# Optimization experiments

Measured on AMD Instinct MI355X. Metric: run time of the kernel, lower is better.

The kernel has to match this reference:

```python
import jax, jax.numpy as jnp
import numpy as np

B = 8            # number of point clouds in the batch
NT = 8192        # target points per cloud
NS = 2048        # source points per cloud
K = 3            # knn_interpolate neighbors
C_TGT = 128      # target (skip) feature channels
C_SRC = 256      # source feature channels
C_IN = C_TGT + C_SRC   # 384 = mlp_channels[0]
C_HID = 256            # mlp_channels[1]
C_OUT = 128            # mlp_channels[2]
EPS = 1e-16


def setup_inputs() -> dict:
    key = jax.random.key(0)
    ks = jax.random.split(key, 10)
    Nt, Ns = B * NT, B * NS
    s1 = 1.0 / np.sqrt(C_IN)
    s2 = 1.0 / np.sqrt(C_HID)
    return {
        "x_target": jax.random.normal(ks[0], (Nt, C_TGT), jnp.float32),
        "pos_target": jax.random.normal(ks[1], (Nt, 3), jnp.float32),
        "batch_target": (jnp.arange(Nt, dtype=jnp.int32) // NT).astype(jnp.int32),
        "x_source": jax.random.normal(ks[2], (Ns, C_SRC), jnp.float32),
        "pos_source": jax.random.normal(ks[3], (Ns, 3), jnp.float32),
        "batch_source": (jnp.arange(Ns, dtype=jnp.int32) // NS).astype(jnp.int32),
        "W1": jax.random.normal(ks[4], (C_IN, C_HID), jnp.float32) * s1,
        "b1": jnp.zeros((C_HID,), jnp.float32),
        "W2": jax.random.normal(ks[5], (C_HID, C_OUT), jnp.float32) * s2,
        "b2": jnp.zeros((C_OUT,), jnp.float32),
        "Ws": jax.random.normal(ks[6], (C_IN, C_OUT), jnp.float32) * s1,
        "bs": jnp.zeros((C_OUT,), jnp.float32),
    }


def _knn_interpolate(x_source, pos_source, pos_target):
    """PyG knn_interpolate with inverse-squared-distance weights.
    Batches are contiguous equal-size blocks -> reshape to [B, N, ...]."""
    pt = pos_target.reshape(B, NT, 3)
    ps = pos_source.reshape(B, NS, 3)
    xs = x_source.reshape(B, NS, C_SRC)
    # squared pairwise distances [B, NT, NS]
    d2 = jnp.sum((pt[:, :, None, :] - ps[:, None, :, :]) ** 2, axis=-1)
    neg, idx = jax.lax.top_k(-d2, K)            # idx: [B, NT, K]
    w = 1.0 / jnp.clip(-neg, EPS)               # inverse squared distance
    gathered = jax.vmap(lambda x, i: x[i])(xs, idx)  # [B, NT, K, C_SRC]
    interp = jnp.sum(w[..., None] * gathered, axis=2) / jnp.sum(w, axis=2)[..., None]
    return interp.reshape(B * NT, C_SRC)


def reference(x_target, pos_target, batch_target, x_source, pos_source,
              batch_source, W1, b1, W2, b2, Ws, bs):
    interpolated = _knn_interpolate(x_source, pos_source, pos_target)
    combined = jnp.concatenate([x_target, interpolated], axis=1)  # [Nt, 384]
    h = jax.nn.relu(combined @ W1 + b1) @ W2 + b2                 # MLP branch
    res = combined @ Ws + bs                                      # shortcut
    return jax.nn.relu(h + res)
```

## Files before the change

kernel.cpp:

```cpp
#include <hip/hip_runtime.h>
#include <hip/hip_bf16.h>

#define B_    8
#define NT_   8192
#define NS_   2048
#define NTOT  (B_ * NT_)
#define CTGT  128
#define CSRC  256
#define CIN   384
#define CHID  256
#define COUT  128

typedef __bf16 bf16x8 __attribute__((ext_vector_type(8)));
typedef float  f32x4  __attribute__((ext_vector_type(4)));
typedef unsigned short u16x8 __attribute__((ext_vector_type(8)));

__device__ inline unsigned short f2bf(float f) {
    unsigned int u = __float_as_uint(f);
    u += 0x7FFF + ((u >> 16) & 1);
    return (unsigned short)(u >> 16);
}

__device__ __forceinline__ void gload16(const unsigned short* g, unsigned short* l) {
    __builtin_amdgcn_global_load_lds(
        (const __attribute__((address_space(1))) unsigned int*)g,
        (__attribute__((address_space(3))) unsigned int*)l, 16, 0, 0);
}

__device__ __forceinline__ void stage_ab(
    const unsigned short* __restrict__ ga, int ldA,
    const unsigned short* __restrict__ gb, int ldB,
    unsigned short* Alds, unsigned short* Blds,
    int k0, int widu, int lane) {
    int rloc = lane >> 2;
    int cswz = ((lane & 3) ^ ((lane >> 3) & 3)) * 8;
#pragma unroll
    for (int i = 0; i < 2; ++i) {
        int c = widu * 2 + i;
        int row = c * 16 + rloc;
        gload16(ga + (size_t)row * ldA + k0 + cswz, Alds + c * 512);
        gload16(gb + (size_t)row * ldB + k0 + cswz, Blds + c * 512);
    }
}

__global__ __launch_bounds__(256) void prep_weights(
    const float* __restrict__ W1, const float* __restrict__ Ws,
    const float* __restrict__ W2,
    unsigned short* __restrict__ Wct, unsigned short* __restrict__ W2t) {
    int g = blockIdx.x * 256 + threadIdx.x;
    if (g < CIN * CIN) {
        int n = g / CIN, k = g % CIN;
        float v = (n < CHID) ? W1[(size_t)k * CHID + n]
                             : Ws[(size_t)k * COUT + (n - CHID)];
        Wct[g] = f2bf(v);
    } else {
        int g2 = g - CIN * CIN;
        if (g2 < COUT * CHID) {
            int n = g2 / CHID, k = g2 % CHID;
            W2t[g2] = f2bf(W2[(size_t)k * COUT + n]);
        }
    }
}

__global__ __launch_bounds__(256) void knn_kernel(
    const float* __restrict__ pos_t, const float* __restrict__ pos_s,
    int* __restrict__ knn_i, float* __restrict__ knn_d) {
    __shared__ float4 ps4[NS_];
    __shared__ float  md[256 * 3];
    __shared__ int    mi[256 * 3];

    int blk = blockIdx.x;
    int batch = blk >> 8;
    const float* src = pos_s + (size_t)batch * NS_ * 3;
    for (int i = threadIdx.x; i < NS_; i += 256) {
        ps4[i] = make_float4(src[i * 3 + 0], src[i * 3 + 1], src[i * 3 + 2], 0.0f);
    }
    __syncthreads();

    int tl = threadIdx.x & 31;
    int ck = threadIdx.x >> 5;
    int t = blk * 32 + tl;
    float ptx = pos_t[t * 3 + 0];
    float pty = pos_t[t * 3 + 1];
    float ptz = pos_t[t * 3 + 2];

    float d0 = 3.4e38f, d1 = 3.4e38f, d2v = 3.4e38f;
    int i0 = 0, i1 = 0, i2 = 0;
    int jbeg = ck * 256, jend = jbeg + 256;
#pragma unroll 4
    for (int j = jbeg; j < jend; ++j) {
        float4 p = ps4[j];
        float dx = __fsub_rn(ptx, p.x);
        float dy = __fsub_rn(pty, p.y);
        float dz = __fsub_rn(ptz, p.z);
        float d = __fadd_rn(__fadd_rn(__fmul_rn(dx, dx), __fmul_rn(dy, dy)),
                            __fmul_rn(dz, dz));
        if (d < d2v) {
            if (d < d1) {
                d2v = d1; i2 = i1;
                if (d < d0) { d1 = d0; i1 = i0; d0 = d; i0 = j; }
                else        { d1 = d;  i1 = j; }
            } else { d2v = d; i2 = j; }
        }
    }
    int slot = (tl * 8 + ck) * 3;
    md[slot + 0] = d0;  md[slot + 1] = d1;  md[slot + 2] = d2v;
    mi[slot + 0] = i0;  mi[slot + 1] = i1;  mi[slot + 2] = i2;
    __syncthreads();

    if (ck == 0) {
        float e0 = md[tl * 24 + 0], e1 = md[tl * 24 + 1], e2 = md[tl * 24 + 2];
        int   j0 = mi[tl * 24 + 0], j1 = mi[tl * 24 + 1], j2 = mi[tl * 24 + 2];
#pragma unroll
        for (int c = 1; c < 8; ++c) {
#pragma unroll
            for (int r = 0; r < 3; ++r) {
                float d = md[tl * 24 + c * 3 + r];
                int   i = mi[tl * 24 + c * 3 + r];
                if (d < e2) {
                    if (d < e1) {
                        e2 = e1; j2 = j1;
                        if (d < e0) { e1 = e0; j1 = j0; e0 = d; j0 = i; }
                        else        { e1 = d;  j1 = i; }
                    } else { e2 = d; j2 = i; }
                }
            }
        }
        knn_i[t * 3 + 0] = j0; knn_i[t * 3 + 1] = j1; knn_i[t * 3 + 2] = j2;
        knn_d[t * 3 + 0] = e0; knn_d[t * 3 + 1] = e1; knn_d[t * 3 + 2] = e2;
    }
}

__global__ __launch_bounds__(256) void interp_kernel(
    const float* __restrict__ x_t, const float* __restrict__ x_s,
    const int* __restrict__ knn_i, const float* __restrict__ knn_d,
    unsigned short* __restrict__ combined) {
    int g = blockIdx.x * 256 + threadIdx.x;
    int row = g / 96, seg = g % 96;
    if (row >= NTOT) return;
    if (seg < 32) {
        float4 v = *(const float4*)(x_t + (size_t)row * CTGT + seg * 4);
        ushort4 o;
        o.x = f2bf(v.x); o.y = f2bf(v.y); o.z = f2bf(v.z); o.w = f2bf(v.w);
        *(ushort4*)(combined + (size_t)row * CIN + seg * 4) = o;
    } else {
        int c = (seg - 32) * 4;
        int batch = row >> 13;
        const float* xsb = x_s + (size_t)batch * NS_ * CSRC;
        int i0 = knn_i[row * 3 + 0];
        int i1 = knn_i[row * 3 + 1];
        int i2 = knn_i[row * 3 + 2];
        float w0 = 1.0f / fmaxf(knn_d[row * 3 + 0], 1e-16f);
        float w1 = 1.0f / fmaxf(knn_d[row * 3 + 1], 1e-16f);
        float w2 = 1.0f / fmaxf(knn_d[row * 3 + 2], 1e-16f);
        float inv = 1.0f / (w0 + w1 + w2);
        float4 a = *(const float4*)(xsb + (size_t)i0 * CSRC + c);
        float4 b = *(const float4*)(xsb + (size_t)i1 * CSRC + c);
        float4 d = *(const float4*)(xsb + (size_t)i2 * CSRC + c);
        ushort4 o;
        o.x = f2bf((w0 * a.x + w1 * b.x + w2 * d.x) * inv);
        o.y = f2bf((w0 * a.y + w1 * b.y + w2 * d.y) * inv);
        o.z = f2bf((w0 * a.z + w1 * b.z + w2 * d.z) * inv);
        o.w = f2bf((w0 * a.w + w1 * b.w + w2 * d.w) * inv);
        *(ushort4*)(combined + (size_t)row * CIN + CTGT + c) = o;
    }
}

__global__ __launch_bounds__(256) void gemm1_kernel(
    const unsigned short* __restrict__ A, const unsigned short* __restrict__ Bt,
    const float* __restrict__ b1, const float* __restrict__ bs,
    unsigned short* __restrict__ hbuf, float* __restrict__ resbuf) {
    __shared__ unsigned short Alds[2][128 * 32];
    __shared__ unsigned short Blds[2][128 * 32];
    int tid = threadIdx.x;
    int wid = tid >> 6, lane = tid & 63;
    int widu = __builtin_amdgcn_readfirstlane(wid);
    int wm = wid >> 1, wn = wid & 1;
    int r = lane & 15, g = lane >> 4;
    int kcol = (g * 8) ^ (((r >> 1) & 3) * 8);

    const unsigned short* ga = A  + (size_t)(blockIdx.x * 128) * CIN;
    const unsigned short* gb = Bt + (size_t)(blockIdx.y * 128) * CIN;

    f32x4 acc[4][4] = {};

    stage_ab(ga, CIN, gb, CIN, Alds[0], Blds[0], 0, widu, lane);
    __syncthreads();
    int cur = 0;
#pragma unroll 1
    for (int t = 0; t < 12; ++t) {
        if (t + 1 < 12)
            stage_ab(ga, CIN, gb, CIN, Alds[cur ^ 1], Blds[cur ^ 1],
                     (t + 1) * 32, widu, lane);
        bf16x8 af[4], bf[4];
#pragma unroll
        for (int mi = 0; mi < 4; ++mi)
            af[mi] = *(const bf16x8*)(&Alds[cur][(wm * 64 + mi * 16 + r) * 32 + kcol]);
#pragma unroll
        for (int ni = 0; ni < 4; ++ni)
            bf[ni] = *(const bf16x8*)(&Blds[cur][(wn * 64 + ni * 16 + r) * 32 + kcol]);
#pragma unroll
        for (int mi = 0; mi < 4; ++mi)
#pragma unroll
            for (int ni = 0; ni < 4; ++ni)
                acc[mi][ni] = __builtin_amdgcn_mfma_f32_16x16x32_bf16(
                    af[mi], bf[ni], acc[mi][ni], 0, 0, 0);
        __syncthreads();
        cur ^= 1;
    }

    int r0 = g * 4;
#pragma unroll
    for (int mi = 0; mi < 4; ++mi)
#pragma unroll
        for (int ni = 0; ni < 4; ++ni) {
            int n = blockIdx.y * 128 + wn * 64 + ni * 16 + r;
#pragma unroll
            for (int rr = 0; rr < 4; ++rr) {
                int m = blockIdx.x * 128 + wm * 64 + mi * 16 + r0 + rr;
                float v = acc[mi][ni][rr];
                if (n < CHID) {
                    v += b1[n];
                    v = fmaxf(v, 0.0f);
                    hbuf[(size_t)m * CHID + n] = f2bf(v);
                } else {
                    int n2 = n - CHID;
                    resbuf[(size_t)m * COUT + n2] = v + bs[n2];
                }
            }
        }
}

__global__ __launch_bounds__(256) void gemm2_kernel(
    const unsigned short* __restrict__ A, const unsigned short* __restrict__ Bt,
    const float* __restrict__ b2, const float* __restrict__ resbuf,
    float* __restrict__ out) {
    __shared__ unsigned short Alds[2][128 * 32];
    __shared__ unsigned short Blds[2][128 * 32];
    int tid = threadIdx.x;
    int wid = tid >> 6, lane = tid & 63;
    int widu = __builtin_amdgcn_readfirstlane(wid);
    int wm = wid >> 1, wn = wid & 1;
    int r = lane & 15, g = lane >> 4;
    int kcol = (g * 8) ^ (((r >> 1) & 3) * 8);

    const unsigned short* ga = A + (size_t)(blockIdx.x * 128) * CHID;

    f32x4 acc[4][4] = {};

    stage_ab(ga, CHID, Bt, CHID, Alds[0], Blds[0], 0, widu, lane);
    __syncthreads();
    int cur = 0;
#pragma unroll 1
    for (int t = 0; t < 8; ++t) {
        if (t + 1 < 8)
            stage_ab(ga, CHID, Bt, CHID, Alds[cur ^ 1], Blds[cur ^ 1],
                     (t + 1) * 32, widu, lane);
        bf16x8 af[4], bf[4];
#pragma unroll
        for (int mi = 0; mi < 4; ++mi)
            af[mi] = *(const bf16x8*)(&Alds[cur][(wm * 64 + mi * 16 + r) * 32 + kcol]);
#pragma unroll
        for (int ni = 0; ni < 4; ++ni)
            bf[ni] = *(const bf16x8*)(&Blds[cur][(wn * 64 + ni * 16 + r) * 32 + kcol]);
#pragma unroll
        for (int mi = 0; mi < 4; ++mi)
#pragma unroll
            for (int ni = 0; ni < 4; ++ni)
                acc[mi][ni] = __builtin_amdgcn_mfma_f32_16x16x32_bf16(
                    af[mi], bf[ni], acc[mi][ni], 0, 0, 0);
        __syncthreads();
        cur ^= 1;
    }

    int r0 = g * 4;
#pragma unroll
    for (int mi = 0; mi < 4; ++mi)
#pragma unroll
        for (int ni = 0; ni < 4; ++ni) {
            int n = wn * 64 + ni * 16 + r;
#pragma unroll
            for (int rr = 0; rr < 4; ++rr) {
                int m = blockIdx.x * 128 + wm * 64 + mi * 16 + r0 + rr;
                float v = acc[mi][ni][rr] + b2[n] + resbuf[(size_t)m * COUT + n];
                out[(size_t)m * COUT + n] = fmaxf(v, 0.0f);
            }
        }
}

extern "C" void kernel_launch(void* const* d_in, const int* in_sizes, int n_in,
                              void* d_out, int out_size, void* d_ws, size_t ws_size,
                              hipStream_t stream) {
    const float* x_t   = (const float*)d_in[0];
    const float* pos_t = (const float*)d_in[1];
    const float* x_s   = (const float*)d_in[3];
    const float* pos_s = (const float*)d_in[4];
    const float* W1    = (const float*)d_in[6];
    const float* b1    = (const float*)d_in[7];
    const float* W2    = (const float*)d_in[8];
    const float* b2    = (const float*)d_in[9];
    const float* Ws    = (const float*)d_in[10];
    const float* bs    = (const float*)d_in[11];

    char* ws = (char*)d_ws;
    int*            knn_i  = (int*)           (ws + 0);
    float*          knn_d  = (float*)         (ws + 786432);
    unsigned short* Wct    = (unsigned short*)(ws + 1572864);
    unsigned short* W2t    = (unsigned short*)(ws + 1867776);
    unsigned short* comb   = (unsigned short*)(ws + 1933312);
    unsigned short* hbuf   = (unsigned short*)(ws + 52264960);
    float*          resbuf = (float*)         (ws + 85819392);
    float*          out    = (float*)d_out;

    prep_weights<<<704, 256, 0, stream>>>(W1, Ws, W2, Wct, W2t);
    knn_kernel<<<NTOT / 32, 256, 0, stream>>>(pos_t, pos_s, knn_i, knn_d);
    interp_kernel<<<(NTOT * 96) / 256, 256, 0, stream>>>(x_t, x_s, knn_i, knn_d, comb);
    dim3 g1(NTOT / 128, CIN / 128);
    gemm1_kernel<<<g1, 256, 0, stream>>>(comb, Wct, b1, bs, hbuf, resbuf);
    gemm2_kernel<<<NTOT / 128, 256, 0, stream>>>(hbuf, W2t, b2, resbuf, out);
}
```

Measured before the change: 275.0 us.

## Fuse both MLP GEMMs into one kernel and make knn branchless with more targets per thread

The two GEMM kernels are merged into one 512-thread kernel. Each block computes the full 384-wide first GEMM for 128 rows, keeps the hidden activations in swizzled LDS, runs the second GEMM from there and adds the shortcut accumulator directly, so the hbuf and resbuf round trips through HBM go away. The knn kernel now handles four targets per thread, reusing each LDS source point load, and replaces its nested branches with branchless fmed3/select insertion. The grid shrinks to 512 blocks with 80KB of dynamic LDS, which risks low occupancy and a short tail, and the knn change raises register pressure.

```diff
diff --git a/kernel.cpp b/kernel.cpp
--- a/kernel.cpp
+++ b/kernel.cpp
@@ -13,7 +13,6 @@
 
 typedef __bf16 bf16x8 __attribute__((ext_vector_type(8)));
 typedef float  f32x4  __attribute__((ext_vector_type(4)));
-typedef unsigned short u16x8 __attribute__((ext_vector_type(8)));
 
 __device__ inline unsigned short f2bf(float f) {
     unsigned int u = __float_as_uint(f);
@@ -25,22 +24,6 @@
     __builtin_amdgcn_global_load_lds(
         (const __attribute__((address_space(1))) unsigned int*)g,
         (__attribute__((address_space(3))) unsigned int*)l, 16, 0, 0);
-}
-
-__device__ __forceinline__ void stage_ab(
-    const unsigned short* __restrict__ ga, int ldA,
-    const unsigned short* __restrict__ gb, int ldB,
-    unsigned short* Alds, unsigned short* Blds,
-    int k0, int widu, int lane) {
-    int rloc = lane >> 2;
-    int cswz = ((lane & 3) ^ ((lane >> 3) & 3)) * 8;
-#pragma unroll
-    for (int i = 0; i < 2; ++i) {
-        int c = widu * 2 + i;
-        int row = c * 16 + rloc;
-        gload16(ga + (size_t)row * ldA + k0 + cswz, Alds + c * 512);
-        gload16(gb + (size_t)row * ldB + k0 + cswz, Blds + c * 512);
-    }
 }
 
 __global__ __launch_bounds__(256) void prep_weights(
@@ -65,12 +48,13 @@
 __global__ __launch_bounds__(256) void knn_kernel(
     const float* __restrict__ pos_t, const float* __restrict__ pos_s,
     int* __restrict__ knn_i, float* __restrict__ knn_d) {
-    __shared__ float4 ps4[NS_];
-    __shared__ float  md[256 * 3];
-    __shared__ int    mi[256 * 3];
+    __shared__ char smem[32768];
+    float4* ps4 = (float4*)smem;
+    float*  md  = (float*)smem;
+    int*    mi  = (int*)(smem + 12288);
 
     int blk = blockIdx.x;
-    int batch = blk >> 8;
+    int batch = blk >> 6;
     const float* src = pos_s + (size_t)batch * NS_ * 3;
     for (int i = threadIdx.x; i < NS_; i += 256) {
         ps4[i] = make_float4(src[i * 3 + 0], src[i * 3 + 1], src[i * 3 + 2], 0.0f);
@@ -79,55 +63,79 @@
 
     int tl = threadIdx.x & 31;
     int ck = threadIdx.x >> 5;
-    int t = blk * 32 + tl;
-    float ptx = pos_t[t * 3 + 0];
-    float pty = pos_t[t * 3 + 1];
-    float ptz = pos_t[t * 3 + 2];
-
-    float d0 = 3.4e38f, d1 = 3.4e38f, d2v = 3.4e38f;
-    int i0 = 0, i1 = 0, i2 = 0;
+    int t0 = blk * 128 + tl;
+    float px[4], py[4], pz[4];
+#pragma unroll
+    for (int q = 0; q < 4; ++q) {
+        px[q] = pos_t[(t0 + q * 32) * 3 + 0];
+        py[q] = pos_t[(t0 + q * 32) * 3 + 1];
+        pz[q] = pos_t[(t0 + q * 32) * 3 + 2];
+    }
+    float e0[4], e1[4], e2[4];
+    int j0[4], j1[4], j2[4];
+#pragma unroll
+    for (int q = 0; q < 4; ++q) {
+        e0[q] = e1[q] = e2[q] = 3.4e38f;
+        j0[q] = j1[q] = j2[q] = 0;
+    }
+
     int jbeg = ck * 256, jend = jbeg + 256;
-#pragma unroll 4
+#pragma unroll 2
     for (int j = jbeg; j < jend; ++j) {
         float4 p = ps4[j];
-        float dx = __fsub_rn(ptx, p.x);
-        float dy = __fsub_rn(pty, p.y);
-        float dz = __fsub_rn(ptz, p.z);
-        float d = __fadd_rn(__fadd_rn(__fmul_rn(dx, dx), __fmul_rn(dy, dy)),
-                            __fmul_rn(dz, dz));
-        if (d < d2v) {
-            if (d < d1) {
-                d2v = d1; i2 = i1;
-                if (d < d0) { d1 = d0; i1 = i0; d0 = d; i0 = j; }
-                else        { d1 = d;  i1 = j; }
-            } else { d2v = d; i2 = j; }
-        }
-    }
-    int slot = (tl * 8 + ck) * 3;
-    md[slot + 0] = d0;  md[slot + 1] = d1;  md[slot + 2] = d2v;
-    mi[slot + 0] = i0;  mi[slot + 1] = i1;  mi[slot + 2] = i2;
-    __syncthreads();
-
-    if (ck == 0) {
-        float e0 = md[tl * 24 + 0], e1 = md[tl * 24 + 1], e2 = md[tl * 24 + 2];
-        int   j0 = mi[tl * 24 + 0], j1 = mi[tl * 24 + 1], j2 = mi[tl * 24 + 2];
+#pragma unroll
+        for (int q = 0; q < 4; ++q) {
+            float dx = __fsub_rn(px[q], p.x);
+            float dy = __fsub_rn(py[q], p.y);
+            float dz = __fsub_rn(pz[q], p.z);
+            float d = __fadd_rn(__fadd_rn(__fmul_rn(dx, dx), __fmul_rn(dy, dy)),
+                                __fmul_rn(dz, dz));
+            bool c0 = d < e0[q], c1 = d < e1[q], c2 = d < e2[q];
+            int n2i = c2 ? (c1 ? j1[q] : j) : j2[q];
+            int n1i = c1 ? (c0 ? j0[q] : j) : j1[q];
+            int n0i = c0 ? j : j0[q];
+            float v2 = __builtin_amdgcn_fmed3f(d, e1[q], e2[q]);
+            float v1 = __builtin_amdgcn_fmed3f(d, e0[q], e1[q]);
+            float v0 = fminf(e0[q], d);
+            e0[q] = v0; e1[q] = v1; e2[q] = v2;
+            j0[q] = n0i; j1[q] = n1i; j2[q] = n2i;
+        }
+    }
+    __syncthreads();
+
+#pragma unroll
+    for (int q = 0; q < 4; ++q) {
+        int slot = ((tl + q * 32) * 8 + ck) * 3;
+        md[slot + 0] = e0[q]; md[slot + 1] = e1[q]; md[slot + 2] = e2[q];
+        mi[slot + 0] = j0[q]; mi[slot + 1] = j1[q]; mi[slot + 2] = j2[q];
+    }
+    __syncthreads();
+
+    if (threadIdx.x < 128) {
+        int tloc = threadIdx.x;
+        int t = blk * 128 + tloc;
+        int base = tloc * 24;
+        float E0 = md[base + 0], E1 = md[base + 1], E2 = md[base + 2];
+        int   J0 = mi[base + 0], J1 = mi[base + 1], J2 = mi[base + 2];
 #pragma unroll
         for (int c = 1; c < 8; ++c) {
 #pragma unroll
-            for (int r = 0; r < 3; ++r) {
-                float d = md[tl * 24 + c * 3 + r];
-                int   i = mi[tl * 24 + c * 3 + r];
-                if (d < e2) {
-                    if (d < e1) {
-                        e2 = e1; j2 = j1;
-                        if (d < e0) { e1 = e0; j1 = j0; e0 = d; j0 = i; }
-                        else        { e1 = d;  j1 = i; }
-                    } else { e2 = d; j2 = i; }
-                }
+            for (int rr = 0; rr < 3; ++rr) {
+                float d = md[base + c * 3 + rr];
+                int   i = mi[base + c * 3 + rr];
+                bool c0 = d < E0, c1 = d < E1, c2 = d < E2;
+                int n2i = c2 ? (c1 ? J1 : i) : J2;
+                int n1i = c1 ? (c0 ? J0 : i) : J1;
+                int n0i = c0 ? i : J0;
+                float ne2 = __builtin_amdgcn_fmed3f(d, E1, E2);
+                float ne1 = __builtin_amdgcn_fmed3f(d, E0, E1);
+                float ne0 = fminf(E0, d);
+                E0 = ne0; E1 = ne1; E2 = ne2;
+                J0 = n0i; J1 = n1i; J2 = n2i;
             }
         }
-        knn_i[t * 3 + 0] = j0; knn_i[t * 3 + 1] = j1; knn_i[t * 3 + 2] = j2;
-        knn_d[t * 3 + 0] = e0; knn_d[t * 3 + 1] = e1; knn_d[t * 3 + 2] = e2;
+        knn_i[t * 3 + 0] = J0; knn_i[t * 3 + 1] = J1; knn_i[t * 3 + 2] = J2;
+        knn_d[t * 3 + 0] = E0; knn_d[t * 3 + 1] = E1; knn_d[t * 3 + 2] = E2;
     }
 }
 
@@ -166,124 +174,124 @@
     }
 }
 
-__global__ __launch_bounds__(256) void gemm1_kernel(
-    const unsigned short* __restrict__ A, const unsigned short* __restrict__ Bt,
+__device__ __forceinline__ void stage1_ld(
+    const unsigned short* __restrict__ ga, const unsigned short* __restrict__ Wct,
+    unsigned short* Asm, unsigned short* Bsm,
+    int k0, int buf, int widu, int rloc, int cswz) {
+    gload16(ga + (size_t)(widu * 16 + rloc) * CIN + k0 + cswz,
+            Asm + buf * 4096 + widu * 512);
+#pragma unroll
+    for (int p = 0; p < 3; ++p)
+        gload16(Wct + (size_t)(p * 128 + widu * 16 + rloc) * CIN + k0 + cswz,
+                Bsm + buf * 12288 + (p * 8 + widu) * 512);
+}
+
+__global__ __launch_bounds__(512) void mlp_fused(
+    const unsigned short* __restrict__ A, const unsigned short* __restrict__ Wct,
+    const unsigned short* __restrict__ W2t,
     const float* __restrict__ b1, const float* __restrict__ bs,
-    unsigned short* __restrict__ hbuf, float* __restrict__ resbuf) {
-    __shared__ unsigned short Alds[2][128 * 32];
-    __shared__ unsigned short Blds[2][128 * 32];
+    const float* __restrict__ b2, float* __restrict__ out) {
+    extern __shared__ char smem[];
+    unsigned short* Asm  = (unsigned short*)smem;
+    unsigned short* Bsm  = (unsigned short*)(smem + 16384);
+    unsigned short* Hsm  = (unsigned short*)smem;
+    unsigned short* B2sm = (unsigned short*)(smem + 65536);
+
     int tid = threadIdx.x;
     int wid = tid >> 6, lane = tid & 63;
     int widu = __builtin_amdgcn_readfirstlane(wid);
-    int wm = wid >> 1, wn = wid & 1;
+    int wm = widu >> 2, wn = widu & 3;
     int r = lane & 15, g = lane >> 4;
     int kcol = (g * 8) ^ (((r >> 1) & 3) * 8);
-
-    const unsigned short* ga = A  + (size_t)(blockIdx.x * 128) * CIN;
-    const unsigned short* gb = Bt + (size_t)(blockIdx.y * 128) * CIN;
-
-    f32x4 acc[4][4] = {};
-
-    stage_ab(ga, CIN, gb, CIN, Alds[0], Blds[0], 0, widu, lane);
+    int rloc = lane >> 2;
+    int cswz = ((lane & 3) ^ ((lane >> 3) & 3)) * 8;
+
+    const unsigned short* ga = A + (size_t)(blockIdx.x * 128) * CIN;
+
+    f32x4 acc[4][6] = {};
+
+    stage1_ld(ga, Wct, Asm, Bsm, 0, 0, widu, rloc, cswz);
     __syncthreads();
     int cur = 0;
 #pragma unroll 1
     for (int t = 0; t < 12; ++t) {
-        if (t + 1 < 12)
-            stage_ab(ga, CIN, gb, CIN, Alds[cur ^ 1], Blds[cur ^ 1],
-                     (t + 1) * 32, widu, lane);
-        bf16x8 af[4], bf[4];
+        if (t + 1 < 12) {
+            stage1_ld(ga, Wct, Asm, Bsm, (t + 1) * 32, cur ^ 1, widu, rloc, cswz);
+        } else {
+            gload16(W2t + (size_t)(widu * 16 + rloc) * CHID + cswz,
+                    B2sm + widu * 512);
+        }
+        bf16x8 af[4], bf[6];
 #pragma unroll
         for (int mi = 0; mi < 4; ++mi)
-            af[mi] = *(const bf16x8*)(&Alds[cur][(wm * 64 + mi * 16 + r) * 32 + kcol]);
-#pragma unroll
-        for (int ni = 0; ni < 4; ++ni)
-            bf[ni] = *(const bf16x8*)(&Blds[cur][(wn * 64 + ni * 16 + r) * 32 + kcol]);
+            af[mi] = *(const bf16x8*)(Asm + cur * 4096 + (wm * 64 + mi * 16 + r) * 32 + kcol);
+#pragma unroll
+        for (int j = 0; j < 6; ++j)
+            bf[j] = *(const bf16x8*)(Bsm + cur * 12288 + (wn * 16 + j * 64 + r) * 32 + kcol);
 #pragma unroll
         for (int mi = 0; mi < 4; ++mi)
 #pragma unroll
-            for (int ni = 0; ni < 4; ++ni)
-                acc[mi][ni] = __builtin_amdgcn_mfma_f32_16x16x32_bf16(
-                    af[mi], bf[ni], acc[mi][ni], 0, 0, 0);
+            for (int j = 0; j < 6; ++j)
+                acc[mi][j] = __builtin_amdgcn_mfma_f32_16x16x32_bf16(
+                    af[mi], bf[j], acc[mi][j], 0, 0, 0);
         __syncthreads();
         cur ^= 1;
     }
 
-    int r0 = g * 4;
 #pragma unroll
     for (int mi = 0; mi < 4; ++mi)
 #pragma unroll
-        for (int ni = 0; ni < 4; ++ni) {
-            int n = blockIdx.y * 128 + wn * 64 + ni * 16 + r;
+        for (int j = 0; j < 4; ++j) {
+            int n = wn * 16 + j * 64 + r;
+            float bb = b1[n];
 #pragma unroll
             for (int rr = 0; rr < 4; ++rr) {
-                int m = blockIdx.x * 128 + wm * 64 + mi * 16 + r0 + rr;
-                float v = acc[mi][ni][rr];
-                if (n < CHID) {
-                    v += b1[n];
-                    v = fmaxf(v, 0.0f);
-                    hbuf[(size_t)m * CHID + n] = f2bf(v);
-                } else {
-                    int n2 = n - CHID;
-                    resbuf[(size_t)m * COUT + n2] = v + bs[n2];
-                }
+                int m = wm * 64 + mi * 16 + g * 4 + rr;
+                float v = fmaxf(acc[mi][j][rr] + bb, 0.0f);
+                int np = (n & ~63) | ((n & 63) ^ ((m & 7) << 3));
+                Hsm[m * 256 + np] = f2bf(v);
             }
         }
-}
-
-__global__ __launch_bounds__(256) void gemm2_kernel(
-    const unsigned short* __restrict__ A, const unsigned short* __restrict__ Bt,
-    const float* __restrict__ b2, const float* __restrict__ resbuf,
-    float* __restrict__ out) {
-    __shared__ unsigned short Alds[2][128 * 32];
-    __shared__ unsigned short Blds[2][128 * 32];
-    int tid = threadIdx.x;
-    int wid = tid >> 6, lane = tid & 63;
-    int widu = __builtin_amdgcn_readfirstlane(wid);
-    int wm = wid >> 1, wn = wid & 1;
-    int r = lane & 15, g = lane >> 4;
-    int kcol = (g * 8) ^ (((r >> 1) & 3) * 8);
-
-    const unsigned short* ga = A + (size_t)(blockIdx.x * 128) * CHID;
-
-    f32x4 acc[4][4] = {};
-
-    stage_ab(ga, CHID, Bt, CHID, Alds[0], Blds[0], 0, widu, lane);
-    __syncthreads();
-    int cur = 0;
+    __syncthreads();
+
+    int cur2 = 0;
 #pragma unroll 1
     for (int t = 0; t < 8; ++t) {
         if (t + 1 < 8)
-            stage_ab(ga, CHID, Bt, CHID, Alds[cur ^ 1], Blds[cur ^ 1],
-                     (t + 1) * 32, widu, lane);
-        bf16x8 af[4], bf[4];
+            gload16(W2t + (size_t)(widu * 16 + rloc) * CHID + (t + 1) * 32 + cswz,
+                    B2sm + (cur2 ^ 1) * 4096 + widu * 512);
+        bf16x8 af2[4], bf2[2];
+#pragma unroll
+        for (int mi = 0; mi < 4; ++mi) {
+            int m = wm * 64 + mi * 16 + r;
+            int c = t * 32 + g * 8;
+            int np = (c & ~63) | ((c & 63) ^ ((m & 7) << 3));
+            af2[mi] = *(const bf16x8*)(Hsm + m * 256 + np);
+        }
+#pragma unroll
+        for (int f = 0; f < 2; ++f)
+            bf2[f] = *(const bf16x8*)(B2sm + cur2 * 4096 + (wn * 16 + f * 64 + r) * 32 + kcol);
 #pragma unroll
         for (int mi = 0; mi < 4; ++mi)
-            af[mi] = *(const bf16x8*)(&Alds[cur][(wm * 64 + mi * 16 + r) * 32 + kcol]);
-#pragma unroll
-        for (int ni = 0; ni < 4; ++ni)
-            bf[ni] = *(const bf16x8*)(&Blds[cur][(wn * 64 + ni * 16 + r) * 32 + kcol]);
-#pragma unroll
-        for (int mi = 0; mi < 4; ++mi)
-#pragma unroll
-            for (int ni = 0; ni < 4; ++ni)
-                acc[mi][ni] = __builtin_amdgcn_mfma_f32_16x16x32_bf16(
-                    af[mi], bf[ni], acc[mi][ni], 0, 0, 0);
+#pragma unroll
+            for (int f = 0; f < 2; ++f)
+                acc[mi][4 + f] = __builtin_amdgcn_mfma_f32_16x16x32_bf16(
+                    af2[mi], bf2[f], acc[mi][4 + f], 0, 0, 0);
         __syncthreads();
-        cur ^= 1;
-    }
-
-    int r0 = g * 4;
+        cur2 ^= 1;
+    }
+
 #pragma unroll
     for (int mi = 0; mi < 4; ++mi)
 #pragma unroll
-        for (int ni = 0; ni < 4; ++ni) {
-            int n = wn * 64 + ni * 16 + r;
+        for (int f = 0; f < 2; ++f) {
+            int n = wn * 16 + f * 64 + r;
+            float bb = b2[n] + bs[n];
 #pragma unroll
             for (int rr = 0; rr < 4; ++rr) {
-                int m = blockIdx.x * 128 + wm * 64 + mi * 16 + r0 + rr;
-                float v = acc[mi][ni][rr] + b2[n] + resbuf[(size_t)m * COUT + n];
-                out[(size_t)m * COUT + n] = fmaxf(v, 0.0f);
+                int m = wm * 64 + mi * 16 + g * 4 + rr;
+                float v = acc[mi][4 + f][rr] + bb;
+                out[(size_t)(blockIdx.x * 128 + m) * COUT + n] = fmaxf(v, 0.0f);
             }
         }
 }
@@ -303,19 +311,18 @@
     const float* bs    = (const float*)d_in[11];
 
     char* ws = (char*)d_ws;
-    int*            knn_i  = (int*)           (ws + 0);
-    float*          knn_d  = (float*)         (ws + 786432);
-    unsigned short* Wct    = (unsigned short*)(ws + 1572864);
-    unsigned short* W2t    = (unsigned short*)(ws + 1867776);
-    unsigned short* comb   = (unsigned short*)(ws + 1933312);
-    unsigned short* hbuf   = (unsigned short*)(ws + 52264960);
-    float*          resbuf = (float*)         (ws + 85819392);
-    float*          out    = (float*)d_out;
+    int*            knn_i = (int*)           (ws + 0);
+    float*          knn_d = (float*)         (ws + 786432);
+    unsigned short* Wct   = (unsigned short*)(ws + 1572864);
+    unsigned short* W2t   = (unsigned short*)(ws + 1867776);
+    unsigned short* comb  = (unsigned short*)(ws + 1933312);
+    float*          out   = (float*)d_out;
+
+    hipFuncSetAttribute((const void*)mlp_fused,
+                        hipFuncAttributeMaxDynamicSharedMemorySize, 81920);
 
     prep_weights<<<704, 256, 0, stream>>>(W1, Ws, W2, Wct, W2t);
-    knn_kernel<<<NTOT / 32, 256, 0, stream>>>(pos_t, pos_s, knn_i, knn_d);
+    knn_kernel<<<NTOT / 128, 256, 0, stream>>>(pos_t, pos_s, knn_i, knn_d);
     interp_kernel<<<(NTOT * 96) / 256, 256, 0, stream>>>(x_t, x_s, knn_i, knn_d, comb);
-    dim3 g1(NTOT / 128, CIN / 128);
-    gemm1_kernel<<<g1, 256, 0, stream>>>(comb, Wct, b1, bs, hbuf, resbuf);
-    gemm2_kernel<<<NTOT / 128, 256, 0, stream>>>(hbuf, W2t, b2, resbuf, out);
-}
+    mlp_fused<<<512, 512, 81920, stream>>>(comb, Wct, W2t, b1, bs, b2, out);
+}
```

After: 262.4 us. 4.6% less time.
